# Kernel optimization log

Hardware: AMD Instinct MI355X
Metric: run time of the kernel (lower is better)

The kernel has to match this reference:

```python
import jax, jax.numpy as jnp
import numpy as np

B, T, D_MODEL, H, DK = 2, 1024, 1024, 16, 64
ADJ_TOPK, PHASE_TOPK, N_STEPS = 128, 128, 4


def _sparse_softmax(scores, k):
    # top-k per row, softmax over the kept entries, zeros elsewhere
    vals, idx = jax.lax.top_k(scores, k)            # (B,h,T,k)
    w = jax.nn.softmax(vals, axis=-1)
    b, h, t, _ = scores.shape
    bi = jnp.arange(b)[:, None, None, None]
    hi = jnp.arange(h)[None, :, None, None]
    ti = jnp.arange(t)[None, None, :, None]
    return jnp.zeros_like(scores).at[bi, hi, ti, idx].set(w)


def _heads(y):
    return y.reshape(B, T, H, DK).transpose(0, 2, 1, 3)  # (B,h,T,d_k)


def setup_inputs() -> dict:
    key = jax.random.key(0)
    ks = jax.random.split(key, 8)
    s = 0.02
    return {
        "x": jax.random.normal(ks[0], (B, T, D_MODEL), jnp.float32),
        "W_Q": jax.random.normal(ks[1], (D_MODEL, D_MODEL), jnp.float32) * s,
        "W_K": jax.random.normal(ks[2], (D_MODEL, D_MODEL), jnp.float32) * s,
        "W_re": jax.random.normal(ks[3], (D_MODEL, D_MODEL), jnp.float32) * s,
        "W_im": jax.random.normal(ks[4], (D_MODEL, D_MODEL), jnp.float32) * s,
        "W_V": jax.random.normal(ks[5], (D_MODEL, D_MODEL), jnp.float32) * s,
        "W_O": jax.random.normal(ks[6], (D_MODEL, D_MODEL), jnp.float32) * s,
        "logit_lam": jnp.float32(0.0),   # sigmoid -> lam=0.5
        "log_alpha": jnp.float32(-3.0),  # matches nn.Parameter init
    }


def reference(x, W_Q, W_K, W_re, W_im, W_V, W_O, logit_lam, log_alpha):
    # --- AdjacencyBuilder: A = sparse_softmax(QK^T/sqrt(dk)) ---
    Q = _heads(x @ W_Q.T)
    K = _heads(x @ W_K.T)
    scores = jnp.einsum('bhtd,bhsd->bhts', Q, K) / np.sqrt(DK).astype(np.float32)
    A = _sparse_softmax(scores, ADJ_TOPK)          # (B,h,T,T)

    # --- PhaseEncoding: D = W_re x + i W_im x (kept as real/imag pair) ---
    Dr = _heads(x @ W_re.T)
    Di = _heads(x @ W_im.T)
    D0r, D0i = Dr, Di

    # --- TopologyPropagation: D <- (1-lam) D + lam A D, n_steps times ---
    lam = jax.nn.sigmoid(logit_lam)
    for _ in range(N_STEPS):
        Dr = (1.0 - lam) * Dr + lam * jnp.einsum('bhts,bhsd->bhtd', A, Dr)
        Di = (1.0 - lam) * Di + lam * jnp.einsum('bhts,bhsd->bhtd', A, Di)
    alpha = jax.nn.sigmoid(log_alpha)
    Dr = Dr + alpha * D0r
    Di = Di + alpha * D0i

    # --- phase sync attention: Re(D_i . conj(D_j)) on unit-normalized D ---
    norm = jnp.maximum(jnp.sqrt(jnp.sum(Dr * Dr + Di * Di, axis=-1, keepdims=True)), 1e-6)
    Ur, Ui = Dr / norm, Di / norm
    phase_sim = (jnp.einsum('bhtd,bhsd->bhts', Ur, Ur)
                 + jnp.einsum('bhtd,bhsd->bhts', Ui, Ui)) * np.sqrt(2.0 * DK).astype(np.float32)
    phase_attn = _sparse_softmax(phase_sim, PHASE_TOPK)

    # --- weighted V sum + output projection ---
    V = _heads(x @ W_V.T)
    out = jnp.einsum('bhts,bhsd->bhtd', phase_attn, V)
    out = out.transpose(0, 2, 1, 3).reshape(B, T, D_MODEL)
    return out @ W_O.T, phase_attn
```

## Files before the change

### kernel.cpp

```cpp
#include <hip/hip_runtime.h>
#include <cstdint>
#include <cstddef>

#define B_  2
#define T_  1024
#define DM  1024
#define H_  16
#define DK_ 64
#define TOPK 128

typedef unsigned short ushort_t;
typedef __attribute__((ext_vector_type(8))) short short8;
typedef __attribute__((ext_vector_type(8))) unsigned short u16x8;
typedef __attribute__((ext_vector_type(4))) float f32x4;

__device__ __forceinline__ unsigned fkey16(unsigned b) {
  return (b & 0x8000u) ? (0xffffu & ~b) : (b | 0x8000u);
}

__device__ __forceinline__ ushort_t f2bf(float f) {
  unsigned u = __float_as_uint(f);
  return (ushort_t)((u + 0x7fffu + ((u >> 16) & 1u)) >> 16);
}
__device__ __forceinline__ float bf2f(ushort_t u) {
  return __uint_as_float((unsigned)u << 16);
}

__device__ __forceinline__ void gload_lds16(const ushort_t* g, ushort_t* l) {
  __builtin_amdgcn_global_load_lds(
      (const __attribute__((address_space(1))) unsigned int*)(const void*)g,
      (__attribute__((address_space(3))) unsigned int*)(void*)l, 16, 0, 0);
}

__global__ __launch_bounds__(256) void cast6_kernel(
    const float* __restrict__ x, const float* __restrict__ wq,
    const float* __restrict__ wk, const float* __restrict__ wre,
    const float* __restrict__ wim, const float* __restrict__ wv,
    ushort_t* __restrict__ xb, ushort_t* __restrict__ w5b) {
  int z = blockIdx.y;
  const float* src; ushort_t* dst; int n4;
  switch (z) {
    case 0: src = x;   dst = xb;                 n4 = 524288; break;
    case 1: src = wq;  dst = w5b;                n4 = 262144; break;
    case 2: src = wk;  dst = w5b + 1048576;      n4 = 262144; break;
    case 3: src = wre; dst = w5b + 2097152;      n4 = 262144; break;
    case 4: src = wim; dst = w5b + 3145728;      n4 = 262144; break;
    default: src = wv; dst = w5b + 4194304;      n4 = 262144; break;
  }
  int i = blockIdx.x * 256 + threadIdx.x;
  if (i < n4) {
    float4 v = ((const float4*)src)[i];
    ushort4 o;
    o.x = f2bf(v.x); o.y = f2bf(v.y); o.z = f2bf(v.z); o.w = f2bf(v.w);
    ((ushort4*)dst)[i] = o;
  }
}

__global__ __launch_bounds__(256) void cast_bf16_kernel(
    const float* __restrict__ in, ushort_t* __restrict__ out, int n4) {
  int i = blockIdx.x * 256 + threadIdx.x;
  if (i < n4) {
    float4 v = ((const float4*)in)[i];
    ushort4 o;
    o.x = f2bf(v.x); o.y = f2bf(v.y); o.z = f2bf(v.z); o.w = f2bf(v.w);
    ((ushort4*)out)[i] = o;
  }
}

template<int KDIM>
__device__ __forceinline__ void gemm_core(
    const ushort_t* __restrict__ Ab, const ushort_t* __restrict__ Bb,
    ushort_t* ldsA, ushort_t* ldsB, int tid, f32x4 acc[4][4]) {
  const int lane = tid & 63, wid = tid >> 6;
  const int wr = (wid >> 1) * 64, wc = (wid & 1) * 64;
  const int l15 = lane & 15, l4 = lane >> 4;
  for (int k0 = 0; k0 < KDIM; k0 += 64) {
    #pragma unroll
    for (int i = 0; i < 4; ++i) {
      int cid = tid + 256 * i;
      int row = cid >> 3, slot = cid & 7;
      int gc = slot ^ (row & 7);
      gload_lds16(&Ab[(size_t)row * KDIM + k0 + gc * 8], &ldsA[cid * 8]);
      gload_lds16(&Bb[(size_t)row * KDIM + k0 + gc * 8], &ldsB[cid * 8]);
    }
    __syncthreads();
    #pragma unroll
    for (int ks = 0; ks < 2; ++ks) {
      short8 af[4], bfr[4];
      #pragma unroll
      for (int m = 0; m < 4; ++m) {
        int r = wr + m * 16 + l15;
        int c = ks * 4 + l4;
        af[m] = *(const short8*)&ldsA[r * 64 + (c ^ (r & 7)) * 8];
      }
      #pragma unroll
      for (int n = 0; n < 4; ++n) {
        int r = wc + n * 16 + l15;
        int c = ks * 4 + l4;
        bfr[n] = *(const short8*)&ldsB[r * 64 + (c ^ (r & 7)) * 8];
      }
      #pragma unroll
      for (int m = 0; m < 4; ++m)
        #pragma unroll
        for (int n = 0; n < 4; ++n)
          acc[m][n] = __builtin_amdgcn_mfma_f32_16x16x32_bf16(
              af[m], bfr[n], acc[m][n], 0, 0, 0);
    }
    __syncthreads();
  }
}

__global__ __launch_bounds__(256) void proj5_mfma(
    const ushort_t* __restrict__ xb, const ushort_t* __restrict__ wb,
    ushort_t* __restrict__ qh_b, ushort_t* __restrict__ kh_b,
    ushort_t* __restrict__ dt0, ushort_t* __restrict__ vt_b) {
  __shared__ ushort_t ldsA[128 * 64];
  __shared__ ushort_t ldsB[128 * 64];
  int tid = threadIdx.x;
  int orig = (blockIdx.x & 7) * 80 + (blockIdx.x >> 3);
  int bx = orig & 7, by = (orig >> 3) & 15, z = orig >> 7;
  const ushort_t* W = wb + (size_t)z * (DM * DM);
  f32x4 acc[4][4];
  #pragma unroll
  for (int m = 0; m < 4; ++m)
    #pragma unroll
    for (int n = 0; n < 4; ++n) acc[m][n] = (f32x4){0.f, 0.f, 0.f, 0.f};
  gemm_core<DM>(xb + (size_t)by * 128 * DM,
                W + (size_t)bx * 128 * DM, ldsA, ldsB, tid, acc);
  const int lane = tid & 63, wid = tid >> 6;
  int row0 = by * 128 + (wid >> 1) * 64 + (lane >> 4) * 4;
  int col0 = bx * 128 + (wid & 1) * 64 + (lane & 15);
  #pragma unroll
  for (int m = 0; m < 4; ++m)
    #pragma unroll
    for (int n = 0; n < 4; ++n)
      #pragma unroll
      for (int j = 0; j < 4; ++j) {
        int nr = row0 + m * 16 + j;
        int mc = col0 + n * 16;
        int b = nr >> 10, t = nr & 1023, h = mc >> 6, d = mc & 63;
        int head = b * H_ + h;
        float v = acc[m][n][j];
        if (z == 0) {
          qh_b[((size_t)head * T_ + t) * DK_ + d] = f2bf(v);
        } else if (z == 1) {
          kh_b[((size_t)head * T_ + t) * DK_ + d] = f2bf(v);
        } else if (z == 4) {
          vt_b[(size_t)head * 65536 + (size_t)d * 1024 + t] = f2bf(v);
        } else {
          int ddofs = (z == 3) ? 64 : 0;
          dt0[(size_t)head * 131072 + (size_t)(d + ddofs) * 1024 + t] = f2bf(v);
        }
      }
}

template<int KDIM>
__global__ __launch_bounds__(256) void score_mfma(
    const ushort_t* __restrict__ A, const ushort_t* __restrict__ Bm,
    ushort_t* __restrict__ Sout, float scale) {
  __shared__ ushort_t ldsA[128 * 64];
  __shared__ ushort_t ldsB[128 * 64];
  int tid = threadIdx.x;
  int orig = (blockIdx.x & 7) * 256 + (blockIdx.x >> 3);
  int bx = orig & 7, by = (orig >> 3) & 7, z = orig >> 6;
  f32x4 acc[4][4];
  #pragma unroll
  for (int m = 0; m < 4; ++m)
    #pragma unroll
    for (int n = 0; n < 4; ++n) acc[m][n] = (f32x4){0.f, 0.f, 0.f, 0.f};
  gemm_core<KDIM>(A + (size_t)z * T_ * KDIM + (size_t)by * 128 * KDIM,
                  Bm + (size_t)z * T_ * KDIM + (size_t)bx * 128 * KDIM,
                  ldsA, ldsB, tid, acc);
  const int lane = tid & 63, wid = tid >> 6;
  int row0 = by * 128 + (wid >> 1) * 64 + (lane >> 4) * 4;
  int col0 = bx * 128 + (wid & 1) * 64 + (lane & 15);
  ushort_t* Sz = Sout + (size_t)z * T_ * T_;
  #pragma unroll
  for (int m = 0; m < 4; ++m)
    #pragma unroll
    for (int n = 0; n < 4; ++n)
      #pragma unroll
      for (int j = 0; j < 4; ++j)
        Sz[(size_t)(row0 + m * 16 + j) * T_ + col0 + n * 16] =
            f2bf(acc[m][n][j] * scale);
}

__device__ __forceinline__ void mfma_64x128_loop(
    const ushort_t* __restrict__ Ah, const ushort_t* __restrict__ Bh,
    ushort_t* ldsA, ushort_t* ldsB, int tid, f32x4 acc[2][4]) {
  const int lane = tid & 63, wid = tid >> 6;
  const int wr = wid >> 1, wc = wid & 1;
  const int l15 = lane & 15, l4 = lane >> 4;
  for (int k0 = 0; k0 < 1024; k0 += 64) {
    #pragma unroll
    for (int i = 0; i < 2; ++i) {
      int cid = tid + 256 * i;
      int rowc = cid >> 3, slot = cid & 7;
      int gc = slot ^ (rowc & 7);
      gload_lds16(&Ah[(size_t)rowc * 1024 + k0 + gc * 8], &ldsA[cid * 8]);
    }
    #pragma unroll
    for (int i = 0; i < 4; ++i) {
      int cid = tid + 256 * i;
      int rowc = cid >> 3, slot = cid & 7;
      int gc = slot ^ (rowc & 7);
      gload_lds16(&Bh[(size_t)rowc * 1024 + k0 + gc * 8], &ldsB[cid * 8]);
    }
    __syncthreads();
    #pragma unroll
    for (int ks = 0; ks < 2; ++ks) {
      short8 af[2], bfr[4];
      #pragma unroll
      for (int m = 0; m < 2; ++m) {
        int r = wr * 32 + m * 16 + l15;
        int c = ks * 4 + l4;
        af[m] = *(const short8*)&ldsA[r * 64 + (c ^ (r & 7)) * 8];
      }
      #pragma unroll
      for (int n = 0; n < 4; ++n) {
        int r = wc * 64 + n * 16 + l15;
        int c = ks * 4 + l4;
        bfr[n] = *(const short8*)&ldsB[r * 64 + (c ^ (r & 7)) * 8];
      }
      #pragma unroll
      for (int m = 0; m < 2; ++m)
        #pragma unroll
        for (int n = 0; n < 4; ++n)
          acc[m][n] = __builtin_amdgcn_mfma_f32_16x16x32_bf16(
              af[m], bfr[n], acc[m][n], 0, 0, 0);
    }
    __syncthreads();
  }
}

__global__ __launch_bounds__(256) void prop_mfma(
    const ushort_t* __restrict__ Ab, const ushort_t* __restrict__ Dsrc,
    ushort_t* __restrict__ Ddst, const float* __restrict__ logit_lam) {
  __shared__ ushort_t ldsA[64 * 64];
  __shared__ ushort_t ldsB[128 * 64];
  int tid = threadIdx.x;
  int orig = (blockIdx.x & 7) * 64 + (blockIdx.x >> 3);
  int bx = orig & 15, hz = orig >> 4;
  const int lane = tid & 63, wid = tid >> 6;
  const int wr = wid >> 1, wc = wid & 1;
  const int l15 = lane & 15, l4 = lane >> 4;
  const ushort_t* Dh = Dsrc + (size_t)hz * 131072;
  f32x4 acc[2][4];
  #pragma unroll
  for (int m = 0; m < 2; ++m)
    #pragma unroll
    for (int n = 0; n < 4; ++n) acc[m][n] = (f32x4){0.f, 0.f, 0.f, 0.f};
  mfma_64x128_loop(Ab + (size_t)hz * 1048576 + (size_t)bx * 64 * 1024,
                   Dh, ldsA, ldsB, tid, acc);
  float lam = 1.f / (1.f + __expf(-logit_lam[0]));
  ushort_t* Dd = Ddst + (size_t)hz * 131072;
  #pragma unroll
  for (int m = 0; m < 2; ++m)
    #pragma unroll
    for (int n = 0; n < 4; ++n)
      #pragma unroll
      for (int j = 0; j < 4; ++j) {
        int t = bx * 64 + wr * 32 + m * 16 + l4 * 4 + j;
        int dd = wc * 64 + n * 16 + l15;
        size_t o = (size_t)dd * 1024 + t;
        float oldv = bf2f(Dh[o]);
        Dd[o] = f2bf((1.f - lam) * oldv + lam * acc[m][n][j]);
      }
}

__global__ __launch_bounds__(256) void prop_final_mfma(
    const ushort_t* __restrict__ Ab, const ushort_t* __restrict__ Dsrc,
    const ushort_t* __restrict__ Dt0, ushort_t* __restrict__ P,
    const float* __restrict__ logit_lam, const float* __restrict__ log_alpha) {
  __shared__ ushort_t ldsA[64 * 64];
  __shared__ ushort_t ldsB[128 * 64];
  __shared__ float sums[4][2][4][4];
  int tid = threadIdx.x;
  int orig = (blockIdx.x & 7) * 64 + (blockIdx.x >> 3);
  int bx = orig & 15, hz = orig >> 4;
  const int lane = tid & 63, wid = tid >> 6;
  const int wr = wid >> 1, wc = wid & 1;
  const int l15 = lane & 15, l4 = lane >> 4;
  const ushort_t* Dh = Dsrc + (size_t)hz * 131072;
  f32x4 acc[2][4];
  #pragma unroll
  for (int m = 0; m < 2; ++m)
    #pragma unroll
    for (int n = 0; n < 4; ++n) acc[m][n] = (f32x4){0.f, 0.f, 0.f, 0.f};
  mfma_64x128_loop(Ab + (size_t)hz * 1048576 + (size_t)bx * 64 * 1024,
                   Dh, ldsA, ldsB, tid, acc);
  float lam = 1.f / (1.f + __expf(-logit_lam[0]));
  float alpha = 1.f / (1.f + __expf(-log_alpha[0]));
  const ushort_t* D0h = Dt0 + (size_t)hz * 131072;
  float F[2][4][4];
  float ssp[2][4];
  #pragma unroll
  for (int m = 0; m < 2; ++m)
    #pragma unroll
    for (int j = 0; j < 4; ++j) {
      int t = bx * 64 + wr * 32 + m * 16 + l4 * 4 + j;
      float s = 0.f;
      #pragma unroll
      for (int n = 0; n < 4; ++n) {
        int dd = wc * 64 + n * 16 + l15;
        size_t o = (size_t)dd * 1024 + t;
        float f = (1.f - lam) * bf2f(Dh[o]) + lam * acc[m][n][j] +
                  alpha * bf2f(D0h[o]);
        F[m][n][j] = f;
        s += f * f;
      }
      #pragma unroll
      for (int off = 1; off < 16; off <<= 1) s += __shfl_xor(s, off);
      ssp[m][j] = s;
    }
  if (l15 == 0) {
    #pragma unroll
    for (int m = 0; m < 2; ++m)
      #pragma unroll
      for (int j = 0; j < 4; ++j)
        sums[wid][m][j][l4] = ssp[m][j];
  }
  __syncthreads();
  ushort_t* Ph = P + (size_t)hz * 1024 * 128;
  #pragma unroll
  for (int m = 0; m < 2; ++m)
    #pragma unroll
    for (int j = 0; j < 4; ++j) {
      float tot = sums[wid][m][j][l4] + sums[wid ^ 1][m][j][l4];
      float ni = 1.f / fmaxf(sqrtf(tot), 1e-6f);
      int t = bx * 64 + wr * 32 + m * 16 + l4 * 4 + j;
      #pragma unroll
      for (int n = 0; n < 4; ++n) {
        int dd = wc * 64 + n * 16 + l15;
        Ph[(size_t)t * 128 + dd] = f2bf(F[m][n][j] * ni);
      }
    }
}

template<int MODE>
__global__ __launch_bounds__(256) void topk16_kernel(
    ushort_t* __restrict__ Sb, float* __restrict__ denseOut) {
  const int tid = threadIdx.x;
  const int lane = tid & 63, wv = tid >> 6;
  const int row = blockIdx.x * 4 + wv;
  ushort_t* Srow = Sb + (size_t)row * 1024;

  float scr[2][8];
  unsigned kk[2][8];
  #pragma unroll
  for (int g = 0; g < 2; ++g) {
    u16x8 v = *(const u16x8*)&Srow[g * 512 + lane * 8];
    #pragma unroll
    for (int e = 0; e < 8; ++e) {
      scr[g][e] = bf2f(v[e]);
      kk[g][e] = fkey16((unsigned)v[e]);
    }
  }

  unsigned prefix = 0, r = TOPK;
  #pragma unroll
  for (int b = 15; b >= 0; --b) {
    unsigned want = (prefix << 1) | 1u;
    unsigned cnt = 0;
    #pragma unroll
    for (int g = 0; g < 2; ++g)
      #pragma unroll
      for (int e = 0; e < 8; ++e)
        cnt += (unsigned)__popcll(__ballot((kk[g][e] >> b) == want));
    if (cnt >= r) prefix = want;
    else { prefix <<= 1; r -= cnt; }
  }
  const unsigned thr = prefix;

  float mx = -3.402823466e38f;
  #pragma unroll
  for (int g = 0; g < 2; ++g)
    #pragma unroll
    for (int e = 0; e < 8; ++e) mx = fmaxf(mx, scr[g][e]);
  #pragma unroll
  for (int off = 1; off < 64; off <<= 1) mx = fmaxf(mx, __shfl_xor(mx, off));

  const unsigned long long below = (1ull << lane) - 1ull;
  unsigned cum = 0;
  float w[2][8];
  float ps = 0.f;
  #pragma unroll
  for (int g = 0; g < 2; ++g) {
    unsigned long long bal[8];
    #pragma unroll
    for (int e = 0; e < 8; ++e) bal[e] = __ballot(kk[g][e] == thr);
    unsigned rb = cum;
    #pragma unroll
    for (int e = 0; e < 8; ++e) rb += (unsigned)__popcll(bal[e] & below);
    unsigned ownPrior = 0;
    #pragma unroll
    for (int e = 0; e < 8; ++e) {
      bool eq = (kk[g][e] == thr);
      bool sel = (kk[g][e] > thr) || (eq && (rb + ownPrior) < r);
      ownPrior += eq ? 1u : 0u;
      float ex = sel ? __expf(scr[g][e] - mx) : 0.f;
      w[g][e] = ex;
      ps += ex;
    }
    #pragma unroll
    for (int e = 0; e < 8; ++e) cum += (unsigned)__popcll(bal[e]);
  }
  float pss = ps;
  #pragma unroll
  for (int off = 1; off < 64; off <<= 1) pss += __shfl_xor(pss, off);
  const float inv = 1.f / pss;

  if (MODE == 0) {
    float* Drow = denseOut + (size_t)row * 1024;
    #pragma unroll
    for (int g = 0; g < 2; ++g) {
      *(float4*)&Drow[g * 512 + lane * 8] =
          make_float4(w[g][0] * inv, w[g][1] * inv, w[g][2] * inv, w[g][3] * inv);
      *(float4*)&Drow[g * 512 + lane * 8 + 4] =
          make_float4(w[g][4] * inv, w[g][5] * inv, w[g][6] * inv, w[g][7] * inv);
    }
  }
  #pragma unroll
  for (int g = 0; g < 2; ++g) {
    u16x8 o;
    #pragma unroll
    for (int e = 0; e < 8; ++e) o[e] = f2bf(w[g][e] * inv);
    *(u16x8*)&Srow[g * 512 + lane * 8] = o;
  }
}

__global__ __launch_bounds__(256) void attnv_mfma(
    const ushort_t* __restrict__ Wb, const ushort_t* __restrict__ Vt,
    ushort_t* __restrict__ attn_b) {
  __shared__ ushort_t ldsA[64 * 64];
  __shared__ ushort_t ldsB[64 * 64];
  int tid = threadIdx.x;
  int orig = (blockIdx.x & 7) * 64 + (blockIdx.x >> 3);
  int bx = orig & 15, hz = orig >> 4;
  const int lane = tid & 63, wid = tid >> 6;
  const int wr = wid >> 1, wc = wid & 1;
  const int l15 = lane & 15, l4 = lane >> 4;
  const ushort_t* Wh = Wb + (size_t)hz * 1048576 + (size_t)bx * 64 * 1024;
  const ushort_t* Vh = Vt + (size_t)hz * 65536;
  f32x4 acc[2][2];
  #pragma unroll
  for (int m = 0; m < 2; ++m)
    #pragma unroll
    for (int n = 0; n < 2; ++n) acc[m][n] = (f32x4){0.f, 0.f, 0.f, 0.f};
  for (int k0 = 0; k0 < 1024; k0 += 64) {
    #pragma unroll
    for (int i = 0; i < 2; ++i) {
      int cid = tid + 256 * i;
      int rowc = cid >> 3, slot = cid & 7;
      int gc = slot ^ (rowc & 7);
      gload_lds16(&Wh[(size_t)rowc * 1024 + k0 + gc * 8], &ldsA[cid * 8]);
    }
    #pragma unroll
    for (int i = 0; i < 2; ++i) {
      int cid = tid + 256 * i;
      int rowc = cid >> 3, slot = cid & 7;
      int gc = slot ^ (rowc & 7);
      gload_lds16(&Vh[(size_t)rowc * 1024 + k0 + gc * 8], &ldsB[cid * 8]);
    }
    __syncthreads();
    #pragma unroll
    for (int ks = 0; ks < 2; ++ks) {
      short8 af[2], bfr[2];
      #pragma unroll
      for (int m = 0; m < 2; ++m) {
        int r = wr * 32 + m * 16 + l15;
        int c = ks * 4 + l4;
        af[m] = *(const short8*)&ldsA[r * 64 + (c ^ (r & 7)) * 8];
      }
      #pragma unroll
      for (int n = 0; n < 2; ++n) {
        int r = wc * 32 + n * 16 + l15;
        int c = ks * 4 + l4;
        bfr[n] = *(const short8*)&ldsB[r * 64 + (c ^ (r & 7)) * 8];
      }
      #pragma unroll
      for (int m = 0; m < 2; ++m)
        #pragma unroll
        for (int n = 0; n < 2; ++n)
          acc[m][n] = __builtin_amdgcn_mfma_f32_16x16x32_bf16(
              af[m], bfr[n], acc[m][n], 0, 0, 0);
    }
    __syncthreads();
  }
  int b = hz >> 4, h = hz & 15;
  #pragma unroll
  for (int m = 0; m < 2; ++m)
    #pragma unroll
    for (int n = 0; n < 2; ++n)
      #pragma unroll
      for (int j = 0; j < 4; ++j) {
        int t = bx * 64 + wr * 32 + m * 16 + l4 * 4 + j;
        int d = wc * 32 + n * 16 + l15;
        attn_b[((size_t)(b * T_ + t)) * DM + h * DK_ + d] = f2bf(acc[m][n][j]);
      }
}

__global__ __launch_bounds__(256) void outproj_mfma(
    const ushort_t* __restrict__ A, const ushort_t* __restrict__ Wo,
    float* __restrict__ out) {
  __shared__ ushort_t ldsA[64 * 64];
  __shared__ ushort_t ldsB[128 * 64];
  int tid = threadIdx.x;
  int orig = (blockIdx.x & 7) * 32 + (blockIdx.x >> 3);
  int bx = orig & 7, by = orig >> 3;
  const int lane = tid & 63, wid = tid >> 6;
  const int wr = wid >> 1, wc = wid & 1;
  const int l15 = lane & 15, l4 = lane >> 4;
  f32x4 acc[2][4];
  #pragma unroll
  for (int m = 0; m < 2; ++m)
    #pragma unroll
    for (int n = 0; n < 4; ++n) acc[m][n] = (f32x4){0.f, 0.f, 0.f, 0.f};
  mfma_64x128_loop(A + (size_t)by * 64 * 1024,
                   Wo + (size_t)bx * 128 * 1024, ldsA, ldsB, tid, acc);
  #pragma unroll
  for (int m = 0; m < 2; ++m)
    #pragma unroll
    for (int n = 0; n < 4; ++n)
      #pragma unroll
      for (int j = 0; j < 4; ++j) {
        int r = by * 64 + wr * 32 + m * 16 + l4 * 4 + j;
        int c = bx * 128 + wc * 64 + n * 16 + l15;
        out[(size_t)r * 1024 + c] = acc[m][n][j];
      }
}

extern "C" void kernel_launch(void* const* d_in, const int* in_sizes, int n_in,
                              void* d_out, int out_size, void* d_ws, size_t ws_size,
                              hipStream_t stream) {
  (void)in_sizes; (void)n_in; (void)out_size; (void)ws_size;
  const float* x         = (const float*)d_in[0];
  const float* wq        = (const float*)d_in[1];
  const float* wk        = (const float*)d_in[2];
  const float* wre       = (const float*)d_in[3];
  const float* wim       = (const float*)d_in[4];
  const float* wv        = (const float*)d_in[5];
  const float* wo        = (const float*)d_in[6];
  const float* logit_lam = (const float*)d_in[7];
  const float* log_alpha = (const float*)d_in[8];

  float* out   = (float*)d_out;
  float* dense = out + (size_t)B_ * T_ * DM;
  ushort_t* w5_b = (ushort_t*)dense;

  char* ws = (char*)d_ws;
  const size_t MB = (size_t)1 << 20;
  ushort_t* A_b  = (ushort_t*)(ws + 0 * MB);
  ushort_t* S2_b = A_b;
  ushort_t* dt0  = (ushort_t*)(ws + 64 * MB);
  ushort_t* dtA  = (ushort_t*)(ws + 72 * MB);
  ushort_t* dtB  = (ushort_t*)(ws + 80 * MB);
  ushort_t* P_b  = dtB;
  ushort_t* vt_b = (ushort_t*)(ws + 88 * MB);
  ushort_t* xb   = (ushort_t*)(ws + 92 * MB);
  ushort_t* attn_b = xb;
  ushort_t* qh_b = (ushort_t*)(ws + 96 * MB);
  ushort_t* wo_b = qh_b;
  ushort_t* kh_b = (ushort_t*)(ws + 100 * MB);

  const int rows = B_ * H_ * T_;

  cast6_kernel<<<dim3(2048, 6), 256, 0, stream>>>(
      x, wq, wk, wre, wim, wv, xb, w5_b);

  proj5_mfma<<<640, 256, 0, stream>>>(xb, w5_b, qh_b, kh_b, dt0, vt_b);

  score_mfma<64><<<2048, 256, 0, stream>>>(qh_b, kh_b, A_b, 0.125f);
  cast_bf16_kernel<<<1024, 256, 0, stream>>>(wo, wo_b, DM * DM / 4);
  topk16_kernel<1><<<rows / 4, 256, 0, stream>>>(A_b, nullptr);

  prop_mfma<<<512, 256, 0, stream>>>(A_b, dt0, dtA, logit_lam);
  prop_mfma<<<512, 256, 0, stream>>>(A_b, dtA, dtB, logit_lam);
  prop_mfma<<<512, 256, 0, stream>>>(A_b, dtB, dtA, logit_lam);
  prop_final_mfma<<<512, 256, 0, stream>>>(A_b, dtA, dt0, P_b,
                                           logit_lam, log_alpha);

  score_mfma<128><<<2048, 256, 0, stream>>>(P_b, P_b, S2_b, 11.3137085f);
  topk16_kernel<0><<<rows / 4, 256, 0, stream>>>(S2_b, dense);

  attnv_mfma<<<512, 256, 0, stream>>>(S2_b, vt_b, attn_b);
  outproj_mfma<<<256, 256, 0, stream>>>(attn_b, wo_b, out);
}
```

Baseline: 342.7 us.

## Exploit symmetry of phase-similarity matrix to compute only upper-triangular tiles

The phase similarity P·Pᵀ is symmetric, so the new kernel computes only the 36 upper-triangular 128x128 tiles per batch-head (1152 blocks instead of 2048). Each off-diagonal tile is written directly, then transposed through swizzled LDS and written to the mirrored position. This roughly halves the MFMA work and operand loads for this stage. The cost is an extra LDS transpose pass and a barrier in off-diagonal blocks, plus uneven per-block work.

```diff
diff --git a/kernel.cpp b/kernel.cpp
--- a/kernel.cpp
+++ b/kernel.cpp
@@ -185,6 +185,62 @@
             f2bf(acc[m][n][j] * scale);
 }
 
+__global__ __launch_bounds__(256) void score_sym_mfma(
+    const ushort_t* __restrict__ P, ushort_t* __restrict__ Sout, float scale) {
+  __shared__ ushort_t lds[128 * 128];
+  ushort_t* ldsA = lds;
+  ushort_t* ldsB = lds + 128 * 64;
+  int tid = threadIdx.x;
+  int swz = (blockIdx.x & 7) * 144 + (blockIdx.x >> 3);
+  int z = swz / 36, t = swz % 36;
+  int by = 0, rem = t;
+  while (rem >= 8 - by) { rem -= 8 - by; ++by; }
+  int bx = by + rem;
+  const ushort_t* Pz = P + (size_t)z * T_ * 128;
+  f32x4 acc[4][4];
+  #pragma unroll
+  for (int m = 0; m < 4; ++m)
+    #pragma unroll
+    for (int n = 0; n < 4; ++n) acc[m][n] = (f32x4){0.f, 0.f, 0.f, 0.f};
+  gemm_core<128>(Pz + (size_t)by * 128 * 128, Pz + (size_t)bx * 128 * 128,
+                 ldsA, ldsB, tid, acc);
+  const int lane = tid & 63, wid = tid >> 6;
+  const int l15 = lane & 15, l4 = lane >> 4;
+  ushort_t* Sz = Sout + (size_t)z * T_ * T_;
+  int row0 = by * 128 + (wid >> 1) * 64 + l4 * 4;
+  int col0 = bx * 128 + (wid & 1) * 64 + l15;
+  #pragma unroll
+  for (int m = 0; m < 4; ++m)
+    #pragma unroll
+    for (int n = 0; n < 4; ++n)
+      #pragma unroll
+      for (int j = 0; j < 4; ++j)
+        Sz[(size_t)(row0 + m * 16 + j) * T_ + col0 + n * 16] =
+            f2bf(acc[m][n][j] * scale);
+  if (bx != by) {
+    int lr0 = (wid >> 1) * 64 + l4 * 4;
+    int lc0 = (wid & 1) * 64 + l15;
+    #pragma unroll
+    for (int m = 0; m < 4; ++m)
+      #pragma unroll
+      for (int n = 0; n < 4; ++n)
+        #pragma unroll
+        for (int j = 0; j < 4; ++j) {
+          int lr = lr0 + m * 16 + j;
+          int lc = lc0 + n * 16;
+          lds[lc * 128 + (lr ^ ((lc & 15) << 3))] = f2bf(acc[m][n][j] * scale);
+        }
+    __syncthreads();
+    int p = tid >> 1, qh = (tid & 1) * 64;
+    int s = (p & 15) << 3;
+    ushort_t* dstRow = Sz + (size_t)(bx * 128 + p) * T_ + by * 128 + qh;
+    #pragma unroll
+    for (int qc = 0; qc < 8; ++qc)
+      *(u16x8*)&dstRow[qc * 8] =
+          *(const u16x8*)&lds[p * 128 + ((qh + qc * 8) ^ s)];
+  }
+}
+
 __device__ __forceinline__ void mfma_64x128_loop(
     const ushort_t* __restrict__ Ah, const ushort_t* __restrict__ Bh,
     ushort_t* ldsA, ushort_t* ldsB, int tid, f32x4 acc[2][4]) {
@@ -580,7 +636,7 @@
   prop_final_mfma<<<512, 256, 0, stream>>>(A_b, dtA, dt0, P_b,
                                            logit_lam, log_alpha);
 
-  score_mfma<128><<<2048, 256, 0, stream>>>(P_b, P_b, S2_b, 11.3137085f);
+  score_sym_mfma<<<1152, 256, 0, stream>>>(P_b, S2_b, 11.3137085f);
   topk16_kernel<0><<<rows / 4, 256, 0, stream>>>(S2_b, dense);
 
   attnv_mfma<<<512, 256, 0, stream>>>(S2_b, vt_b, attn_b);
```

Result: no change. 336.7 us (-1.8%).
